# Kernel tuning notes

Measured on AMD Instinct MI355X. Metric: run time of the kernel, lower is better.

## Reference

```python
import jax, jax.numpy as jnp
import numpy as np

HIDDEN = 512
KEY_DIM = HIDDEN // 8  # 64
B, N, M = 8, 2048, 2048


def setup_inputs() -> dict:
    key = jax.random.key(0)
    kx, ky, kwq, kbq, kwk, kbk = jax.random.split(key, 6)
    s = 1.0 / np.sqrt(HIDDEN)
    return {
        "x": jax.random.normal(kx, (B, N, HIDDEN), dtype=jnp.float32),
        "y": jax.random.normal(ky, (B, M, HIDDEN), dtype=jnp.float32),
        "Wq": jax.random.uniform(kwq, (KEY_DIM, HIDDEN), minval=-s, maxval=s, dtype=jnp.float32),
        "bq": jax.random.uniform(kbq, (KEY_DIM,), minval=-s, maxval=s, dtype=jnp.float32),
        "Wk": jax.random.uniform(kwk, (KEY_DIM, HIDDEN), minval=-s, maxval=s, dtype=jnp.float32),
        "bk": jax.random.uniform(kbk, (KEY_DIM,), minval=-s, maxval=s, dtype=jnp.float32),
    }


def reference(x, y, Wq, bq, Wk, bk):
    # linear projections (torch Linear: x @ W^T + b)
    q = jnp.einsum("bnh,kh->bnk", x, Wq) + bq  # [B,N,K]
    k = jnp.einsum("bmh,kh->bmk", y, Wk) + bk  # [B,M,K]
    # pairwise squared distance [B,N,M]
    dist = (
        -2.0 * jnp.einsum("bnk,bmk->bnm", q, k)
        + jnp.sum(q * q, axis=-1)[:, :, None]
        + jnp.sum(k * k, axis=-1)[:, None, :]
    )
    # max over M of exp(-dist), keepdim -> [B,N,1]
    atweight = jnp.max(jnp.exp(-dist), axis=-1, keepdims=True)
    # outer product per batch -> [B,N,N]
    attention = jnp.einsum("bni,bmi->bnm", atweight, atweight)
    return attention
```

## Files before the change

### kernel.cpp

```cpp
#include <hip/hip_runtime.h>

#define B_    8
#define N_    2048
#define H_    512
#define K_    64
#define NROWS 16384
#define RTOT  32768

typedef __attribute__((ext_vector_type(8))) __bf16 bf16x8;
typedef __attribute__((ext_vector_type(4))) float  floatx4;

#define MFMA(a, b, c) __builtin_amdgcn_mfma_f32_16x16x32_bf16((a), (b), (c), 0, 0, 0)

__global__ __launch_bounds__(256) void wcvt_kernel(
    const float* __restrict__ Wq, const float* __restrict__ Wk,
    __bf16* __restrict__ Whilo)
{
    const int i = blockIdx.x * 256 + threadIdx.x;
    const bool isQ = i < 32768;
    const int off = isQ ? i : i - 32768;
    const float f = isQ ? Wq[off] : Wk[off];
    const __bf16 h = (__bf16)f;
    const __bf16 l = (__bf16)(f - (float)h);
    const int base = isQ ? 0 : 65536;
    Whilo[base + off] = h;
    Whilo[base + 32768 + off] = l;
}

__global__ __launch_bounds__(128) void proj_kernel(
    const float* __restrict__ x, const float* __restrict__ y,
    const __bf16* __restrict__ Whilo,
    const float* __restrict__ bq, const float* __restrict__ bk,
    __bf16* __restrict__ qh, __bf16* __restrict__ ql,
    float* __restrict__ sq)
{
    const int tid  = threadIdx.x;
    const int wv   = tid >> 6;
    const int lane = tid & 63;
    const int quad = lane >> 4;
    const int l16  = lane & 15;
    const int rowbase = blockIdx.x * 64 + wv * 32;
    const bool isQ = rowbase < NROWS;
    const float* __restrict__ X   = isQ ? x : y;
    const int xrow0 = isQ ? rowbase : rowbase - NROWS;
    const __bf16* __restrict__ Whi = Whilo + (isQ ? 0 : 2 * 32768);
    const __bf16* __restrict__ Wlo = Whi + 32768;
    const float* __restrict__ bias = isQ ? bq : bk;

    floatx4 acc[2][4];
    #pragma unroll
    for (int rt = 0; rt < 2; ++rt)
        #pragma unroll
        for (int ot = 0; ot < 4; ++ot)
            acc[rt][ot] = floatx4{0.f, 0.f, 0.f, 0.f};

    for (int it = 0; it < 16; ++it) {
        const int k0 = it * 32 + quad * 8;
        bf16x8 ahi[2], alo[2];
        #pragma unroll
        for (int rt = 0; rt < 2; ++rt) {
            const float4 f0 = *reinterpret_cast<const float4*>(
                &X[(size_t)(xrow0 + rt * 16 + l16) * H_ + k0]);
            const float4 f1 = *reinterpret_cast<const float4*>(
                &X[(size_t)(xrow0 + rt * 16 + l16) * H_ + k0 + 4]);
            const float fv[8] = {f0.x, f0.y, f0.z, f0.w, f1.x, f1.y, f1.z, f1.w};
            #pragma unroll
            for (int j = 0; j < 8; ++j) {
                const __bf16 h = (__bf16)fv[j];
                ahi[rt][j] = h;
                alo[rt][j] = (__bf16)(fv[j] - (float)h);
            }
        }
        bf16x8 bhi[4], blo[4];
        #pragma unroll
        for (int ot = 0; ot < 4; ++ot) {
            const int wrow = ot * 16 + l16;
            bhi[ot] = *reinterpret_cast<const bf16x8*>(&Whi[(size_t)wrow * H_ + k0]);
            blo[ot] = *reinterpret_cast<const bf16x8*>(&Wlo[(size_t)wrow * H_ + k0]);
        }
        #pragma unroll
        for (int rt = 0; rt < 2; ++rt)
            #pragma unroll
            for (int ot = 0; ot < 4; ++ot) {
                acc[rt][ot] = MFMA(ahi[rt], bhi[ot], acc[rt][ot]);
                acc[rt][ot] = MFMA(ahi[rt], blo[ot], acc[rt][ot]);
                acc[rt][ot] = MFMA(alo[rt], bhi[ot], acc[rt][ot]);
            }
    }

    float bv[4];
    #pragma unroll
    for (int ot = 0; ot < 4; ++ot) bv[ot] = bias[ot * 16 + l16];

    #pragma unroll
    for (int rt = 0; rt < 2; ++rt) {
        float ss[4] = {0.f, 0.f, 0.f, 0.f};
        #pragma unroll
        for (int ot = 0; ot < 4; ++ot)
            #pragma unroll
            for (int r = 0; r < 4; ++r) {
                const float qv = acc[rt][ot][r] + bv[ot];
                acc[rt][ot][r] = qv;
                ss[r] = fmaf(qv, qv, ss[r]);
            }
        #pragma unroll
        for (int off = 1; off < 16; off <<= 1)
            #pragma unroll
            for (int r = 0; r < 4; ++r)
                ss[r] += __shfl_xor(ss[r], off);
        const int row0 = rowbase + rt * 16 + quad * 4;
        if (l16 == 0) {
            #pragma unroll
            for (int r = 0; r < 4; ++r) sq[row0 + r] = ss[r];
        }
        #pragma unroll
        for (int ot = 0; ot < 4; ++ot)
            #pragma unroll
            for (int r = 0; r < 4; ++r) {
                const size_t idx = (size_t)(row0 + r) * K_ + ot * 16 + l16;
                const float qv = acc[rt][ot][r];
                const __bf16 h = (__bf16)qv;
                qh[idx] = h;
                ql[idx] = (__bf16)(qv - (float)h);
            }
    }
}

__global__ __launch_bounds__(128) void dist_kernel(
    const __bf16* __restrict__ qh, const __bf16* __restrict__ ql,
    const float* __restrict__ sq, float* __restrict__ wout)
{
    const int tid  = threadIdx.x;
    const int wv   = tid >> 6;
    const int lane = tid & 63;
    const int quad = lane >> 4;
    const int l16  = lane & 15;
    const int blk  = blockIdx.x;
    const int b    = blk >> 6;
    const int nrow = (blk & 63) * 32 + wv * 16;
    const size_t qrow = (size_t)(b * N_ + nrow + l16);

    const bf16x8 ahi0 = *reinterpret_cast<const bf16x8*>(&qh[qrow * K_ + quad * 8]);
    const bf16x8 ahi1 = *reinterpret_cast<const bf16x8*>(&qh[qrow * K_ + 32 + quad * 8]);
    const bf16x8 alo0 = *reinterpret_cast<const bf16x8*>(&ql[qrow * K_ + quad * 8]);
    const bf16x8 alo1 = *reinterpret_cast<const bf16x8*>(&ql[qrow * K_ + 32 + quad * 8]);

    const __bf16* __restrict__ kh = qh + (size_t)NROWS * K_;
    const __bf16* __restrict__ kl = ql + (size_t)NROWS * K_;
    const float*  __restrict__ kk = sq + NROWS;

    floatx4 runmin = floatx4{1e30f, 1e30f, 1e30f, 1e30f};

    #pragma unroll 2
    for (int ms = 0; ms < 128; ++ms) {
        const size_t krow = (size_t)(b * N_ + ms * 16 + l16);
        const bf16x8 bh0 = *reinterpret_cast<const bf16x8*>(&kh[krow * K_ + quad * 8]);
        const bf16x8 bh1 = *reinterpret_cast<const bf16x8*>(&kh[krow * K_ + 32 + quad * 8]);
        const bf16x8 bl0 = *reinterpret_cast<const bf16x8*>(&kl[krow * K_ + quad * 8]);
        const bf16x8 bl1 = *reinterpret_cast<const bf16x8*>(&kl[krow * K_ + 32 + quad * 8]);
        const float kkv = kk[b * N_ + ms * 16 + l16];

        floatx4 acc = floatx4{0.f, 0.f, 0.f, 0.f};
        acc = MFMA(ahi0, bh0, acc);
        acc = MFMA(ahi1, bh1, acc);
        acc = MFMA(ahi0, bl0, acc);
        acc = MFMA(ahi1, bl1, acc);
        acc = MFMA(alo0, bh0, acc);
        acc = MFMA(alo1, bh1, acc);

        #pragma unroll
        for (int r = 0; r < 4; ++r) {
            const float d = fmaf(-2.f, acc[r], kkv);
            runmin[r] = fminf(runmin[r], d);
        }
    }

    #pragma unroll
    for (int off = 1; off < 16; off <<= 1)
        #pragma unroll
        for (int r = 0; r < 4; ++r)
            runmin[r] = fminf(runmin[r], __shfl_xor(runmin[r], off));

    if (l16 == 0) {
        #pragma unroll
        for (int r = 0; r < 4; ++r) {
            const int row = nrow + quad * 4 + r;
            const float d = runmin[r] + sq[b * N_ + row];
            wout[b * N_ + row] = expf(-d);
        }
    }
}

__global__ __launch_bounds__(256) void outer_kernel(
    const float* __restrict__ w, float4* __restrict__ out)
{
    const int f = blockIdx.x * 256 + threadIdx.x;
    const int m4 = f & 511;
    const int n  = (f >> 9) & 2047;
    const int b  = f >> 20;
    const float wn = w[(b << 11) + n];
    const float4 wm = reinterpret_cast<const float4*>(w)[(b << 9) + m4];
    float4 o;
    o.x = wn * wm.x; o.y = wn * wm.y; o.z = wn * wm.z; o.w = wn * wm.w;
    out[f] = o;
}

extern "C" void kernel_launch(void* const* d_in, const int* in_sizes, int n_in,
                              void* d_out, int out_size, void* d_ws, size_t ws_size,
                              hipStream_t stream)
{
    const float* x  = (const float*)d_in[0];
    const float* y  = (const float*)d_in[1];
    const float* Wq = (const float*)d_in[2];
    const float* bq = (const float*)d_in[3];
    const float* Wk = (const float*)d_in[4];
    const float* bk = (const float*)d_in[5];
    float* out = (float*)d_out;

    char* ws = (char*)d_ws;
    __bf16* qh    = (__bf16*)ws;
    __bf16* ql    = (__bf16*)(ws + 4194304);
    float*  sq    = (float*)(ws + 8388608);
    __bf16* Whilo = (__bf16*)(ws + 8519680);
    float*  w     = (float*)(ws + 8781824);

    wcvt_kernel<<<256, 256, 0, stream>>>(Wq, Wk, Whilo);
    proj_kernel<<<512, 128, 0, stream>>>(x, y, Whilo, bq, bk, qh, ql, sq);
    dist_kernel<<<512, 128, 0, stream>>>(qh, ql, sq, w);
    outer_kernel<<<32768, 256, 0, stream>>>(w, (float4*)out);
}
```

Before: 263.8 us.

## Split distance min over M segments and re-tile projection for more waves

The distance kernel now splits the M dimension into 8 segments, and each wave handles 32 query rows instead of 16, reusing each loaded key tile across two MFMA row tiles. Partial minima are written to a workspace and reduced in a new combine kernel that applies the exp. The projection kernel uses 16 rows per wave with 4 waves per block and software-prefetches the next x chunk. This raises parallelism and occupancy for the serial distance loop at the cost of an extra launch and a small partial-min buffer.

```diff
diff --git a/kernel.cpp b/kernel.cpp
--- a/kernel.cpp
+++ b/kernel.cpp
@@ -5,7 +5,7 @@
 #define H_    512
 #define K_    64
 #define NROWS 16384
-#define RTOT  32768
+#define SEGS  8
 
 typedef __attribute__((ext_vector_type(8))) __bf16 bf16x8;
 typedef __attribute__((ext_vector_type(4))) float  floatx4;
@@ -27,7 +27,7 @@
     Whilo[base + 32768 + off] = l;
 }
 
-__global__ __launch_bounds__(128) void proj_kernel(
+__global__ __launch_bounds__(256) void proj_kernel(
     const float* __restrict__ x, const float* __restrict__ y,
     const __bf16* __restrict__ Whilo,
     const float* __restrict__ bq, const float* __restrict__ bk,
@@ -39,120 +39,123 @@
     const int lane = tid & 63;
     const int quad = lane >> 4;
     const int l16  = lane & 15;
-    const int rowbase = blockIdx.x * 64 + wv * 32;
+    const int rowbase = blockIdx.x * 64 + wv * 16;
     const bool isQ = rowbase < NROWS;
     const float* __restrict__ X   = isQ ? x : y;
-    const int xrow0 = isQ ? rowbase : rowbase - NROWS;
+    const int xrow = (isQ ? rowbase : rowbase - NROWS) + l16;
     const __bf16* __restrict__ Whi = Whilo + (isQ ? 0 : 2 * 32768);
     const __bf16* __restrict__ Wlo = Whi + 32768;
     const float* __restrict__ bias = isQ ? bq : bk;
-
-    floatx4 acc[2][4];
-    #pragma unroll
-    for (int rt = 0; rt < 2; ++rt)
-        #pragma unroll
-        for (int ot = 0; ot < 4; ++ot)
-            acc[rt][ot] = floatx4{0.f, 0.f, 0.f, 0.f};
+    const float* __restrict__ Xr = X + (size_t)xrow * H_;
+
+    floatx4 acc[4];
+    #pragma unroll
+    for (int ot = 0; ot < 4; ++ot)
+        acc[ot] = floatx4{0.f, 0.f, 0.f, 0.f};
+
+    float4 f0 = *reinterpret_cast<const float4*>(&Xr[quad * 8]);
+    float4 f1 = *reinterpret_cast<const float4*>(&Xr[quad * 8 + 4]);
 
     for (int it = 0; it < 16; ++it) {
+        const int nk0 = (it < 15 ? it + 1 : it) * 32 + quad * 8;
+        const float4 nf0 = *reinterpret_cast<const float4*>(&Xr[nk0]);
+        const float4 nf1 = *reinterpret_cast<const float4*>(&Xr[nk0 + 4]);
+
+        const float fv[8] = {f0.x, f0.y, f0.z, f0.w, f1.x, f1.y, f1.z, f1.w};
+        bf16x8 ahi, alo;
+        #pragma unroll
+        for (int j = 0; j < 8; ++j) {
+            const __bf16 h = (__bf16)fv[j];
+            ahi[j] = h;
+            alo[j] = (__bf16)(fv[j] - (float)h);
+        }
+
         const int k0 = it * 32 + quad * 8;
-        bf16x8 ahi[2], alo[2];
-        #pragma unroll
-        for (int rt = 0; rt < 2; ++rt) {
-            const float4 f0 = *reinterpret_cast<const float4*>(
-                &X[(size_t)(xrow0 + rt * 16 + l16) * H_ + k0]);
-            const float4 f1 = *reinterpret_cast<const float4*>(
-                &X[(size_t)(xrow0 + rt * 16 + l16) * H_ + k0 + 4]);
-            const float fv[8] = {f0.x, f0.y, f0.z, f0.w, f1.x, f1.y, f1.z, f1.w};
-            #pragma unroll
-            for (int j = 0; j < 8; ++j) {
-                const __bf16 h = (__bf16)fv[j];
-                ahi[rt][j] = h;
-                alo[rt][j] = (__bf16)(fv[j] - (float)h);
-            }
-        }
-        bf16x8 bhi[4], blo[4];
         #pragma unroll
         for (int ot = 0; ot < 4; ++ot) {
             const int wrow = ot * 16 + l16;
-            bhi[ot] = *reinterpret_cast<const bf16x8*>(&Whi[(size_t)wrow * H_ + k0]);
-            blo[ot] = *reinterpret_cast<const bf16x8*>(&Wlo[(size_t)wrow * H_ + k0]);
-        }
-        #pragma unroll
-        for (int rt = 0; rt < 2; ++rt)
-            #pragma unroll
-            for (int ot = 0; ot < 4; ++ot) {
-                acc[rt][ot] = MFMA(ahi[rt], bhi[ot], acc[rt][ot]);
-                acc[rt][ot] = MFMA(ahi[rt], blo[ot], acc[rt][ot]);
-                acc[rt][ot] = MFMA(alo[rt], bhi[ot], acc[rt][ot]);
-            }
+            const bf16x8 bhi = *reinterpret_cast<const bf16x8*>(&Whi[(size_t)wrow * H_ + k0]);
+            const bf16x8 blo = *reinterpret_cast<const bf16x8*>(&Wlo[(size_t)wrow * H_ + k0]);
+            acc[ot] = MFMA(ahi, bhi, acc[ot]);
+            acc[ot] = MFMA(ahi, blo, acc[ot]);
+            acc[ot] = MFMA(alo, bhi, acc[ot]);
+        }
+        f0 = nf0; f1 = nf1;
     }
 
     float bv[4];
     #pragma unroll
     for (int ot = 0; ot < 4; ++ot) bv[ot] = bias[ot * 16 + l16];
 
-    #pragma unroll
-    for (int rt = 0; rt < 2; ++rt) {
-        float ss[4] = {0.f, 0.f, 0.f, 0.f};
-        #pragma unroll
-        for (int ot = 0; ot < 4; ++ot)
-            #pragma unroll
-            for (int r = 0; r < 4; ++r) {
-                const float qv = acc[rt][ot][r] + bv[ot];
-                acc[rt][ot][r] = qv;
-                ss[r] = fmaf(qv, qv, ss[r]);
-            }
-        #pragma unroll
-        for (int off = 1; off < 16; off <<= 1)
-            #pragma unroll
-            for (int r = 0; r < 4; ++r)
-                ss[r] += __shfl_xor(ss[r], off);
-        const int row0 = rowbase + rt * 16 + quad * 4;
-        if (l16 == 0) {
-            #pragma unroll
-            for (int r = 0; r < 4; ++r) sq[row0 + r] = ss[r];
-        }
-        #pragma unroll
-        for (int ot = 0; ot < 4; ++ot)
-            #pragma unroll
-            for (int r = 0; r < 4; ++r) {
-                const size_t idx = (size_t)(row0 + r) * K_ + ot * 16 + l16;
-                const float qv = acc[rt][ot][r];
-                const __bf16 h = (__bf16)qv;
-                qh[idx] = h;
-                ql[idx] = (__bf16)(qv - (float)h);
-            }
-    }
-}
-
-__global__ __launch_bounds__(128) void dist_kernel(
+    float ss[4] = {0.f, 0.f, 0.f, 0.f};
+    #pragma unroll
+    for (int ot = 0; ot < 4; ++ot)
+        #pragma unroll
+        for (int r = 0; r < 4; ++r) {
+            const float qv = acc[ot][r] + bv[ot];
+            acc[ot][r] = qv;
+            ss[r] = fmaf(qv, qv, ss[r]);
+        }
+    #pragma unroll
+    for (int off = 1; off < 16; off <<= 1)
+        #pragma unroll
+        for (int r = 0; r < 4; ++r)
+            ss[r] += __shfl_xor(ss[r], off);
+
+    const int row0 = rowbase + quad * 4;
+    if (l16 == 0) {
+        #pragma unroll
+        for (int r = 0; r < 4; ++r) sq[row0 + r] = ss[r];
+    }
+    #pragma unroll
+    for (int ot = 0; ot < 4; ++ot)
+        #pragma unroll
+        for (int r = 0; r < 4; ++r) {
+            const size_t idx = (size_t)(row0 + r) * K_ + ot * 16 + l16;
+            const float qv = acc[ot][r];
+            const __bf16 h = (__bf16)qv;
+            qh[idx] = h;
+            ql[idx] = (__bf16)(qv - (float)h);
+        }
+}
+
+__global__ __launch_bounds__(256, 4) void dist_kernel(
     const __bf16* __restrict__ qh, const __bf16* __restrict__ ql,
-    const float* __restrict__ sq, float* __restrict__ wout)
+    const float* __restrict__ sq, float* __restrict__ pmin)
 {
     const int tid  = threadIdx.x;
     const int wv   = tid >> 6;
     const int lane = tid & 63;
     const int quad = lane >> 4;
     const int l16  = lane & 15;
-    const int blk  = blockIdx.x;
-    const int b    = blk >> 6;
-    const int nrow = (blk & 63) * 32 + wv * 16;
-    const size_t qrow = (size_t)(b * N_ + nrow + l16);
-
-    const bf16x8 ahi0 = *reinterpret_cast<const bf16x8*>(&qh[qrow * K_ + quad * 8]);
-    const bf16x8 ahi1 = *reinterpret_cast<const bf16x8*>(&qh[qrow * K_ + 32 + quad * 8]);
-    const bf16x8 alo0 = *reinterpret_cast<const bf16x8*>(&ql[qrow * K_ + quad * 8]);
-    const bf16x8 alo1 = *reinterpret_cast<const bf16x8*>(&ql[qrow * K_ + 32 + quad * 8]);
+    const int wid  = blockIdx.x * 4 + wv;
+    const int rg   = wid & 511;
+    const int seg  = wid >> 9;
+    const int b    = rg >> 6;
+    const int nrow = (rg & 63) * 32;
+    const size_t qbase = (size_t)(b * N_ + nrow);
+
+    bf16x8 ahi[2][2], alo[2][2];
+    #pragma unroll
+    for (int rt = 0; rt < 2; ++rt) {
+        const size_t qrow = qbase + rt * 16 + l16;
+        ahi[rt][0] = *reinterpret_cast<const bf16x8*>(&qh[qrow * K_ + quad * 8]);
+        ahi[rt][1] = *reinterpret_cast<const bf16x8*>(&qh[qrow * K_ + 32 + quad * 8]);
+        alo[rt][0] = *reinterpret_cast<const bf16x8*>(&ql[qrow * K_ + quad * 8]);
+        alo[rt][1] = *reinterpret_cast<const bf16x8*>(&ql[qrow * K_ + 32 + quad * 8]);
+    }
 
     const __bf16* __restrict__ kh = qh + (size_t)NROWS * K_;
     const __bf16* __restrict__ kl = ql + (size_t)NROWS * K_;
     const float*  __restrict__ kk = sq + NROWS;
 
-    floatx4 runmin = floatx4{1e30f, 1e30f, 1e30f, 1e30f};
-
+    floatx4 runmin[2];
+    runmin[0] = floatx4{1e30f, 1e30f, 1e30f, 1e30f};
+    runmin[1] = floatx4{1e30f, 1e30f, 1e30f, 1e30f};
+
+    const int msEnd = seg * 16 + 16;
     #pragma unroll 2
-    for (int ms = 0; ms < 128; ++ms) {
+    for (int ms = seg * 16; ms < msEnd; ++ms) {
         const size_t krow = (size_t)(b * N_ + ms * 16 + l16);
         const bf16x8 bh0 = *reinterpret_cast<const bf16x8*>(&kh[krow * K_ + quad * 8]);
         const bf16x8 bh1 = *reinterpret_cast<const bf16x8*>(&kh[krow * K_ + 32 + quad * 8]);
@@ -160,35 +163,57 @@
         const bf16x8 bl1 = *reinterpret_cast<const bf16x8*>(&kl[krow * K_ + 32 + quad * 8]);
         const float kkv = kk[b * N_ + ms * 16 + l16];
 
-        floatx4 acc = floatx4{0.f, 0.f, 0.f, 0.f};
-        acc = MFMA(ahi0, bh0, acc);
-        acc = MFMA(ahi1, bh1, acc);
-        acc = MFMA(ahi0, bl0, acc);
-        acc = MFMA(ahi1, bl1, acc);
-        acc = MFMA(alo0, bh0, acc);
-        acc = MFMA(alo1, bh1, acc);
+        floatx4 a0 = floatx4{0.f, 0.f, 0.f, 0.f};
+        floatx4 a1 = floatx4{0.f, 0.f, 0.f, 0.f};
+        a0 = MFMA(ahi[0][0], bh0, a0);
+        a1 = MFMA(ahi[1][0], bh0, a1);
+        a0 = MFMA(ahi[0][1], bh1, a0);
+        a1 = MFMA(ahi[1][1], bh1, a1);
+        a0 = MFMA(ahi[0][0], bl0, a0);
+        a1 = MFMA(ahi[1][0], bl0, a1);
+        a0 = MFMA(ahi[0][1], bl1, a0);
+        a1 = MFMA(ahi[1][1], bl1, a1);
+        a0 = MFMA(alo[0][0], bh0, a0);
+        a1 = MFMA(alo[1][0], bh0, a1);
+        a0 = MFMA(alo[0][1], bh1, a0);
+        a1 = MFMA(alo[1][1], bh1, a1);
 
         #pragma unroll
         for (int r = 0; r < 4; ++r) {
-            const float d = fmaf(-2.f, acc[r], kkv);
-            runmin[r] = fminf(runmin[r], d);
+            runmin[0][r] = fminf(runmin[0][r], fmaf(-2.f, a0[r], kkv));
+            runmin[1][r] = fminf(runmin[1][r], fmaf(-2.f, a1[r], kkv));
         }
     }
 
     #pragma unroll
     for (int off = 1; off < 16; off <<= 1)
         #pragma unroll
-        for (int r = 0; r < 4; ++r)
-            runmin[r] = fminf(runmin[r], __shfl_xor(runmin[r], off));
+        for (int rt = 0; rt < 2; ++rt)
+            #pragma unroll
+            for (int r = 0; r < 4; ++r)
+                runmin[rt][r] = fminf(runmin[rt][r], __shfl_xor(runmin[rt][r], off));
 
     if (l16 == 0) {
         #pragma unroll
-        for (int r = 0; r < 4; ++r) {
-            const int row = nrow + quad * 4 + r;
-            const float d = runmin[r] + sq[b * N_ + row];
-            wout[b * N_ + row] = expf(-d);
-        }
-    }
+        for (int rt = 0; rt < 2; ++rt)
+            #pragma unroll
+            for (int r = 0; r < 4; ++r) {
+                const int row = nrow + rt * 16 + quad * 4 + r;
+                pmin[(size_t)(b * N_ + row) * SEGS + seg] = runmin[rt][r];
+            }
+    }
+}
+
+__global__ __launch_bounds__(256) void combine_kernel(
+    const float* __restrict__ pmin, const float* __restrict__ sq,
+    float* __restrict__ w)
+{
+    const int i = blockIdx.x * 256 + threadIdx.x;
+    const float4 a = reinterpret_cast<const float4*>(pmin)[i * 2];
+    const float4 c = reinterpret_cast<const float4*>(pmin)[i * 2 + 1];
+    const float m = fminf(fminf(fminf(a.x, a.y), fminf(a.z, a.w)),
+                          fminf(fminf(c.x, c.y), fminf(c.z, c.w)));
+    w[i] = expf(-(m + sq[i]));
 }
 
 __global__ __launch_bounds__(256) void outer_kernel(
@@ -223,9 +248,11 @@
     float*  sq    = (float*)(ws + 8388608);
     __bf16* Whilo = (__bf16*)(ws + 8519680);
     float*  w     = (float*)(ws + 8781824);
+    float*  pmin  = (float*)(ws + 8847360);
 
     wcvt_kernel<<<256, 256, 0, stream>>>(Wq, Wk, Whilo);
-    proj_kernel<<<512, 128, 0, stream>>>(x, y, Whilo, bq, bk, qh, ql, sq);
-    dist_kernel<<<512, 128, 0, stream>>>(qh, ql, sq, w);
+    proj_kernel<<<512, 256, 0, stream>>>(x, y, Whilo, bq, bk, qh, ql, sq);
+    dist_kernel<<<1024, 256, 0, stream>>>(qh, ql, sq, pmin);
+    combine_kernel<<<64, 256, 0, stream>>>(pmin, sq, w);
     outer_kernel<<<32768, 256, 0, stream>>>(w, (float4*)out);
 }
```

Result: faster. 253.3 us (-4.0%).
